# Kernel tuning notes

Hardware: AMD Instinct MI355X
Metric: run time of the kernel (lower is better)

Reference implementation:

```python
import jax, jax.numpy as jnp
import numpy as np

ALPHA = 0.2  # leaky-relu negative slope
N_NODES = 50000
IN_F = 256
OUT_F = 64
N_EDGES = 1600000


def setup_inputs() -> dict:
    key = jax.random.key(0)
    k1, k2, k3, k4 = jax.random.split(key, 4)
    x = jax.random.normal(k1, (N_NODES, IN_F), dtype=jnp.float32)
    # xavier_normal-ish scales for params
    W = jax.random.normal(k2, (IN_F, OUT_F), dtype=jnp.float32) * (1.414 * (2.0 / (IN_F + OUT_F)) ** 0.5)
    a = jax.random.normal(k3, (1, 2 * OUT_F), dtype=jnp.float32) * (1.414 * (2.0 / (1 + 2 * OUT_F)) ** 0.5)
    edge_index = jax.random.randint(k4, (2, N_EDGES), 0, N_NODES, dtype=jnp.int64)
    return {"x": x, "W": W, "a": a, "edge_index": edge_index}


def reference(x, W, a, edge_index):
    N = x.shape[0]
    src = edge_index[0]  # row index of sparse adjacency (aggregation target)
    dst = edge_index[1]  # column index (neighbor being gathered)
    h = x @ W  # [N, out]
    out_f = h.shape[1]
    # a @ cat(h[src], h[dst]) == (h @ a1)[src] + (h @ a2)[dst]
    a1 = a[0, :out_f]
    a2 = a[0, out_f:]
    s_src = h @ a1  # [N]
    s_dst = h @ a2  # [N]
    score = s_src[src] + s_dst[dst]  # [E]
    edge_e = jnp.exp(-jax.nn.leaky_relu(score, negative_slope=ALPHA))  # [E]
    # e_rowsum[i] = sum_{e: src==i} edge_e[e]
    e_rowsum = jax.ops.segment_sum(edge_e, src, num_segments=N)  # [N]
    # h_prime[i] = sum_{e: src==i} edge_e[e] * h[dst[e]]
    h_prime = jax.ops.segment_sum(edge_e[:, None] * h[dst], src, num_segments=N)  # [N, out]
    h_prime = h_prime / e_rowsum[:, None]
    return jax.nn.elu(h_prime)
```

## Files before the change

### kernel.cpp

```cpp
#include <hip/hip_runtime.h>
#include <hip/hip_bf16.h>
#include <hip/hip_fp16.h>


#define ALPHA 0.2f
#define KDIM 256
#define FDIM 64
#define BIN_CHUNK 8192
#define BUCKET_CAP 4096

typedef __bf16 bf16x8 __attribute__((ext_vector_type(8)));
typedef float f32x4 __attribute__((ext_vector_type(4)));
typedef unsigned int u32;
typedef unsigned short u16;

__global__ __launch_bounds__(256) void gat_wt_kernel(
    const float* __restrict__ W, __hip_bfloat16* __restrict__ w_t)
{
    const int t = blockIdx.x * 256 + threadIdx.x;
    if (t < KDIM * FDIM) {
        const int k = t >> 6;
        const int n = t & 63;
        w_t[n * KDIM + k] = __float2bfloat16(W[t]);
    }
}

__global__ __launch_bounds__(256) void gat_gemm_kernel(
    const float* __restrict__ x, const __hip_bfloat16* __restrict__ w_tp,
    const float* __restrict__ a, __hip_bfloat16* __restrict__ h_bf,
    float* __restrict__ s_src, float* __restrict__ s_dst, int N)
{
    const int lane = threadIdx.x & 63;
    const int wv = threadIdx.x >> 6;
    const int m0 = blockIdx.x * 128 + wv * 32;
    const int c = lane & 15;
    const int q = lane >> 4;

    const int r0 = m0 + c;
    const int r1 = m0 + 16 + c;
    const float* xp0 = x + (long)(r0 < N ? r0 : N - 1) * KDIM;
    const float* xp1 = x + (long)(r1 < N ? r1 : N - 1) * KDIM;
    const __bf16* wt = (const __bf16*)w_tp;

    f32x4 acc[2][4];
#pragma unroll
    for (int rt = 0; rt < 2; ++rt)
#pragma unroll
        for (int ct = 0; ct < 4; ++ct) acc[rt][ct] = (f32x4){0.f, 0.f, 0.f, 0.f};

#pragma unroll 2
    for (int kc = 0; kc < 8; ++kc) {
        const int k0 = kc * 32 + q * 8;
        const float4 xa0 = *(const float4*)(xp0 + k0);
        const float4 xb0 = *(const float4*)(xp0 + k0 + 4);
        const float4 xa1 = *(const float4*)(xp1 + k0);
        const float4 xb1 = *(const float4*)(xp1 + k0 + 4);
        bf16x8 af0, af1;
        af0[0] = (__bf16)xa0.x; af0[1] = (__bf16)xa0.y;
        af0[2] = (__bf16)xa0.z; af0[3] = (__bf16)xa0.w;
        af0[4] = (__bf16)xb0.x; af0[5] = (__bf16)xb0.y;
        af0[6] = (__bf16)xb0.z; af0[7] = (__bf16)xb0.w;
        af1[0] = (__bf16)xa1.x; af1[1] = (__bf16)xa1.y;
        af1[2] = (__bf16)xa1.z; af1[3] = (__bf16)xa1.w;
        af1[4] = (__bf16)xb1.x; af1[5] = (__bf16)xb1.y;
        af1[6] = (__bf16)xb1.z; af1[7] = (__bf16)xb1.w;
#pragma unroll
        for (int ct = 0; ct < 4; ++ct) {
            const bf16x8 bf = *(const bf16x8*)(wt + (ct * 16 + c) * KDIM + k0);
            acc[0][ct] = __builtin_amdgcn_mfma_f32_16x16x32_bf16(af0, bf, acc[0][ct], 0, 0, 0);
            acc[1][ct] = __builtin_amdgcn_mfma_f32_16x16x32_bf16(af1, bf, acc[1][ct], 0, 0, 0);
        }
    }

    float a1c[4], a2c[4];
#pragma unroll
    for (int ct = 0; ct < 4; ++ct) {
        a1c[ct] = a[ct * 16 + c];
        a2c[ct] = a[FDIM + ct * 16 + c];
    }

#pragma unroll
    for (int rt = 0; rt < 2; ++rt) {
        const int mb = m0 + rt * 16;
        float s1r[4], s2r[4];
#pragma unroll
        for (int reg = 0; reg < 4; ++reg) {
            float s1 = 0.f, s2 = 0.f;
#pragma unroll
            for (int ct = 0; ct < 4; ++ct) {
                s1 += acc[rt][ct][reg] * a1c[ct];
                s2 += acc[rt][ct][reg] * a2c[ct];
            }
            s1r[reg] = s1; s2r[reg] = s2;
        }
#pragma unroll
        for (int off = 1; off < 16; off <<= 1) {
#pragma unroll
            for (int reg = 0; reg < 4; ++reg) {
                s1r[reg] += __shfl_xor(s1r[reg], off);
                s2r[reg] += __shfl_xor(s2r[reg], off);
            }
        }
#pragma unroll
        for (int reg = 0; reg < 4; ++reg) {
            const int row = mb + q * 4 + reg;
            if (row < N) {
#pragma unroll
                for (int ct = 0; ct < 4; ++ct)
                    h_bf[(long)row * FDIM + ct * 16 + c] = __float2bfloat16(acc[rt][ct][reg]);
                if (c == 0) { s_src[row] = s1r[reg]; s_dst[row] = s2r[reg]; }
            }
        }
    }
}

__global__ __launch_bounds__(256) void gat_bin_kernel(
    const int* __restrict__ srcA, const int* __restrict__ dstA,
    int* __restrict__ bcur, u32* __restrict__ pair, int E, int NBU)
{
    __shared__ int hist[1024];
    __shared__ int lcur[1024];
    const int t = threadIdx.x;
    for (int j = t; j < 1024; j += 256) hist[j] = 0;
    __syncthreads();
    const int base = blockIdx.x * BIN_CHUNK;
    const int cnt = min(BIN_CHUNK, E - base);
    for (int i = t; i < cnt; i += 256)
        atomicAdd(&hist[srcA[base + i] >> 6], 1);
    __syncthreads();
    for (int j = t; j < NBU; j += 256) {
        const int v = hist[j];
        lcur[j] = v ? (j * BUCKET_CAP + atomicAdd(&bcur[j], v)) : 0;
    }
    __syncthreads();
    for (int i = t; i < cnt; i += 256) {
        const int s = srcA[base + i];
        const int d = dstA[base + i];
        const int pos = atomicAdd(&lcur[s >> 6], 1);
        pair[pos] = ((u32)(s & 63) << 16) | (u32)d;
    }
}

__global__ __launch_bounds__(256) void gat_bsort_kernel(
    const u32* __restrict__ pair, const int* __restrict__ bcur,
    const float* __restrict__ s_src, const float* __restrict__ s_dst,
    int* __restrict__ nstart, int* __restrict__ nend,
    u32* __restrict__ sorted_pk, int N)
{
    __shared__ u32 chunk[BUCKET_CAP];
    __shared__ int cur[64];
    __shared__ float ssl[64];

    const int b = blockIdx.x;
    const int t = threadIdx.x;
    const int s0 = b << 6;
    const int abase = b * BUCKET_CAP;
    const int n = min(bcur[b], BUCKET_CAP);

    if (t < 64) {
        cur[t] = 0;
        ssl[t] = (s0 + t < N) ? s_src[s0 + t] : 0.f;
    }
    __syncthreads();
    for (int i = t; i < n; i += 256) {
        const u32 p = pair[abase + i];
        chunk[i] = p;
        atomicAdd(&cur[p >> 16], 1);
    }
    __syncthreads();
    if (t < 64) {
        const int v = cur[t];
        int incl = v;
#pragma unroll
        for (int off = 1; off < 64; off <<= 1) {
            const int nv = __shfl_up(incl, off);
            if (t >= off) incl += nv;
        }
        const int excl = incl - v;
        if (s0 + t < N) {
            nstart[s0 + t] = abase + excl;
            nend[s0 + t] = abase + excl + v;
        }
        cur[t] = excl;
    }
    __syncthreads();
    for (int i = t; i < n; i += 256) {
        const u32 p = chunk[i];
        const int sl = p >> 16;
        const int d = (int)(p & 0xFFFFu);
        const int slot = atomicAdd(&cur[sl], 1);
        const float sc = ssl[sl] + s_dst[d];
        const float lr = sc > 0.f ? sc : ALPHA * sc;
        const float wgt = __expf(-lr);
        const u32 wh = (u32)__half_as_ushort(__float2half(wgt));
        sorted_pk[abase + slot] = (u32)d | (wh << 16);
    }
}

__global__ __launch_bounds__(256) void gat_gather_kernel(
    const int* __restrict__ nstart, const int* __restrict__ nend,
    const u32* __restrict__ sorted_pk,
    const __hip_bfloat16* __restrict__ h_bf, float* __restrict__ out, int N)
{
    const int node = blockIdx.x * 4 + (threadIdx.x >> 6);
    if (node >= N) return;
    const int lane = threadIdx.x & 63;
    const int q = lane >> 3;
    const int c = lane & 7;

    const int start = nstart[node];
    const int end = nend[node];
    const __bf16* hb = (const __bf16*)h_bf;

    float acc0[8], acc1[8];
#pragma unroll
    for (int j = 0; j < 8; ++j) { acc0[j] = 0.f; acc1[j] = 0.f; }
    float wsum0 = 0.f, wsum1 = 0.f;

    int e = start + q;
    for (; e + 8 < end; e += 16) {
        const u32 p0 = sorted_pk[e];
        const u32 p1 = sorted_pk[e + 8];
        const int d0 = (int)(p0 & 0xFFFFu);
        const int d1 = (int)(p1 & 0xFFFFu);
        const bf16x8 hv0 = *(const bf16x8*)(hb + (long)d0 * FDIM + 8 * c);
        const bf16x8 hv1 = *(const bf16x8*)(hb + (long)d1 * FDIM + 8 * c);
        const float w0 = __half2float(__ushort_as_half((u16)(p0 >> 16)));
        const float w1 = __half2float(__ushort_as_half((u16)(p1 >> 16)));
#pragma unroll
        for (int j = 0; j < 8; ++j) {
            acc0[j] += w0 * (float)hv0[j];
            acc1[j] += w1 * (float)hv1[j];
        }
        wsum0 += w0;
        wsum1 += w1;
    }
    if (e < end) {
        const u32 p0 = sorted_pk[e];
        const int d0 = (int)(p0 & 0xFFFFu);
        const bf16x8 hv0 = *(const bf16x8*)(hb + (long)d0 * FDIM + 8 * c);
        const float w0 = __half2float(__ushort_as_half((u16)(p0 >> 16)));
#pragma unroll
        for (int j = 0; j < 8; ++j) acc0[j] += w0 * (float)hv0[j];
        wsum0 += w0;
    }

    float acc[8];
#pragma unroll
    for (int j = 0; j < 8; ++j) acc[j] = acc0[j] + acc1[j];
    float wsum = wsum0 + wsum1;

#pragma unroll
    for (int off = 8; off < 64; off <<= 1) {
#pragma unroll
        for (int j = 0; j < 8; ++j) acc[j] += __shfl_xor(acc[j], off);
        wsum += __shfl_xor(wsum, off);
    }

    if (q == 0) {
        const float inv = 1.0f / wsum;
        float o[8];
#pragma unroll
        for (int j = 0; j < 8; ++j) {
            const float v = acc[j] * inv;
            o[j] = v > 0.f ? v : expm1f(v);
        }
        float* op = &out[(long)node * FDIM + 8 * c];
        *(float4*)op = make_float4(o[0], o[1], o[2], o[3]);
        *(float4*)(op + 4) = make_float4(o[4], o[5], o[6], o[7]);
    }
}

extern "C" void kernel_launch(void* const* d_in, const int* in_sizes, int n_in,
                              void* d_out, int out_size, void* d_ws, size_t ws_size,
                              hipStream_t stream) {
    const float* x = (const float*)d_in[0];
    const float* W = (const float*)d_in[1];
    const float* a = (const float*)d_in[2];
    const int* ei  = (const int*)d_in[3];

    const int N = in_sizes[0] / KDIM;
    const int E = in_sizes[3] / 2;
    const int NBU = (N + 63) >> 6;
    const int NBLK = (E + BIN_CHUNK - 1) / BIN_CHUNK;
    const int* srcA = ei;
    const int* dstA = ei + E;

    __hip_bfloat16* h_bf = (__hip_bfloat16*)d_ws;
    __hip_bfloat16* w_t  = h_bf + (size_t)N * FDIM;
    float* s_src = (float*)(w_t + KDIM * FDIM);
    float* s_dst = s_src + N;
    int* nstart  = (int*)(s_dst + N);
    int* nend    = nstart + N;
    int* bcur    = nend + N;
    u32* pair    = (u32*)(bcur + 1024);
    u32* sorted_pk = pair + (size_t)NBU * BUCKET_CAP;
    float* out   = (float*)d_out;

    hipMemsetAsync(bcur, 0, 1024 * sizeof(int), stream);

    gat_wt_kernel<<<dim3((KDIM * FDIM + 255) / 256), dim3(256), 0, stream>>>(W, w_t);
    gat_gemm_kernel<<<dim3((N + 127) / 128), dim3(256), 0, stream>>>(
        x, w_t, a, h_bf, s_src, s_dst, N);

    gat_bin_kernel<<<dim3(NBLK), dim3(256), 0, stream>>>(srcA, dstA, bcur, pair, E, NBU);
    gat_bsort_kernel<<<dim3(NBU), dim3(256), 0, stream>>>(
        pair, bcur, s_src, s_dst, nstart, nend, sorted_pk, N);

    gat_gather_kernel<<<dim3((N + 3) / 4), dim3(256), 0, stream>>>(
        nstart, nend, sorted_pk, h_bf, out, N);
}
```

Before: 190.1 us.

## Merge edge binning into GEMM launch and fold bucket-counter reset into weight transpose

The separate edge-binning kernel is merged into the GEMM kernel as extra leading blocks, so binning and the projection GEMM run concurrently in one launch. The hipMemsetAsync of the bucket counters is replaced by zeroing inside the weight-transpose kernel, which removes a launch. BIN_CHUNK is halved so there are more binning blocks, raising parallelism at the cost of more global atomics on the bucket counters. The GEMM blocks now reserve the binning kernel's 8 KB of shared memory, which may lower their occupancy.

```diff
diff --git a/kernel.cpp b/kernel.cpp
--- a/kernel.cpp
+++ b/kernel.cpp
@@ -6,7 +6,7 @@
 #define ALPHA 0.2f
 #define KDIM 256
 #define FDIM 64
-#define BIN_CHUNK 8192
+#define BIN_CHUNK 4096
 #define BUCKET_CAP 4096
 
 typedef __bf16 bf16x8 __attribute__((ext_vector_type(8)));
@@ -15,7 +15,8 @@
 typedef unsigned short u16;
 
 __global__ __launch_bounds__(256) void gat_wt_kernel(
-    const float* __restrict__ W, __hip_bfloat16* __restrict__ w_t)
+    const float* __restrict__ W, __hip_bfloat16* __restrict__ w_t,
+    int* __restrict__ bcur)
 {
     const int t = blockIdx.x * 256 + threadIdx.x;
     if (t < KDIM * FDIM) {
@@ -23,16 +24,48 @@
         const int n = t & 63;
         w_t[n * KDIM + k] = __float2bfloat16(W[t]);
     }
-}
-
-__global__ __launch_bounds__(256) void gat_gemm_kernel(
+    if (t < 1024) bcur[t] = 0;
+}
+
+__global__ __launch_bounds__(256) void gat_gemm_bin_kernel(
     const float* __restrict__ x, const __hip_bfloat16* __restrict__ w_tp,
     const float* __restrict__ a, __hip_bfloat16* __restrict__ h_bf,
-    float* __restrict__ s_src, float* __restrict__ s_dst, int N)
+    float* __restrict__ s_src, float* __restrict__ s_dst,
+    const int* __restrict__ srcA, const int* __restrict__ dstA,
+    int* __restrict__ bcur, u32* __restrict__ pair,
+    int N, int E, int NBU, int NBLK)
 {
-    const int lane = threadIdx.x & 63;
-    const int wv = threadIdx.x >> 6;
-    const int m0 = blockIdx.x * 128 + wv * 32;
+    __shared__ int hist[1024];
+    __shared__ int lcur[1024];
+
+    const int t = threadIdx.x;
+
+    if ((int)blockIdx.x < NBLK) {
+        for (int j = t; j < 1024; j += 256) hist[j] = 0;
+        __syncthreads();
+        const int base = blockIdx.x * BIN_CHUNK;
+        const int cnt = min(BIN_CHUNK, E - base);
+        for (int i = t; i < cnt; i += 256)
+            atomicAdd(&hist[srcA[base + i] >> 6], 1);
+        __syncthreads();
+        for (int j = t; j < NBU; j += 256) {
+            const int v = hist[j];
+            lcur[j] = v ? (j * BUCKET_CAP + atomicAdd(&bcur[j], v)) : 0;
+        }
+        __syncthreads();
+        for (int i = t; i < cnt; i += 256) {
+            const int s = srcA[base + i];
+            const int d = dstA[base + i];
+            const int pos = atomicAdd(&lcur[s >> 6], 1);
+            pair[pos] = ((u32)(s & 63) << 16) | (u32)d;
+        }
+        return;
+    }
+
+    const int gb = (int)blockIdx.x - NBLK;
+    const int lane = t & 63;
+    const int wv = t >> 6;
+    const int m0 = gb * 128 + wv * 32;
     const int c = lane & 15;
     const int q = lane >> 4;
 
@@ -114,33 +147,6 @@
     }
 }
 
-__global__ __launch_bounds__(256) void gat_bin_kernel(
-    const int* __restrict__ srcA, const int* __restrict__ dstA,
-    int* __restrict__ bcur, u32* __restrict__ pair, int E, int NBU)
-{
-    __shared__ int hist[1024];
-    __shared__ int lcur[1024];
-    const int t = threadIdx.x;
-    for (int j = t; j < 1024; j += 256) hist[j] = 0;
-    __syncthreads();
-    const int base = blockIdx.x * BIN_CHUNK;
-    const int cnt = min(BIN_CHUNK, E - base);
-    for (int i = t; i < cnt; i += 256)
-        atomicAdd(&hist[srcA[base + i] >> 6], 1);
-    __syncthreads();
-    for (int j = t; j < NBU; j += 256) {
-        const int v = hist[j];
-        lcur[j] = v ? (j * BUCKET_CAP + atomicAdd(&bcur[j], v)) : 0;
-    }
-    __syncthreads();
-    for (int i = t; i < cnt; i += 256) {
-        const int s = srcA[base + i];
-        const int d = dstA[base + i];
-        const int pos = atomicAdd(&lcur[s >> 6], 1);
-        pair[pos] = ((u32)(s & 63) << 16) | (u32)d;
-    }
-}
-
 __global__ __launch_bounds__(256) void gat_bsort_kernel(
     const u32* __restrict__ pair, const int* __restrict__ bcur,
     const float* __restrict__ s_src, const float* __restrict__ s_dst,
@@ -283,6 +289,7 @@
     const int E = in_sizes[3] / 2;
     const int NBU = (N + 63) >> 6;
     const int NBLK = (E + BIN_CHUNK - 1) / BIN_CHUNK;
+    const int GB = (N + 127) / 128;
     const int* srcA = ei;
     const int* dstA = ei + E;
 
@@ -297,13 +304,12 @@
     u32* sorted_pk = pair + (size_t)NBU * BUCKET_CAP;
     float* out   = (float*)d_out;
 
-    hipMemsetAsync(bcur, 0, 1024 * sizeof(int), stream);
-
-    gat_wt_kernel<<<dim3((KDIM * FDIM + 255) / 256), dim3(256), 0, stream>>>(W, w_t);
-    gat_gemm_kernel<<<dim3((N + 127) / 128), dim3(256), 0, stream>>>(
-        x, w_t, a, h_bf, s_src, s_dst, N);
-
-    gat_bin_kernel<<<dim3(NBLK), dim3(256), 0, stream>>>(srcA, dstA, bcur, pair, E, NBU);
+    gat_wt_kernel<<<dim3((KDIM * FDIM + 255) / 256), dim3(256), 0, stream>>>(
+        W, w_t, bcur);
+
+    gat_gemm_bin_kernel<<<dim3(NBLK + GB), dim3(256), 0, stream>>>(
+        x, w_t, a, h_bf, s_src, s_dst, srcA, dstA, bcur, pair, N, E, NBU, NBLK);
+
     gat_bsort_kernel<<<dim3(NBU), dim3(256), 0, stream>>>(
         pair, bcur, s_src, s_dst, nstart, nend, sorted_pk, N);
 
```

After: 172.5 us. 9.2% less time.
